# Performance work log

Hardware: AMD Instinct MI355X
Metric: run time of the kernel (lower is better)

The kernel has to match this reference:

```python
import jax, jax.numpy as jnp
import numpy as np

B, C, D, H, W = 4, 128, 24, 24, 24
P = 64


def _sparse_table(x):
    # Range-max sparse table along the last axis: level k holds max over
    # windows [i, i+2^k). Levels 0..3 (window sizes 1,2,4,8) suffice because
    # adaptive-pool region lengths are ceil(n/2) <= 12 for crop length n <= 24.
    tabs = [x]
    for k in range(1, 4):
        h = 1 << (k - 1)
        prev = tabs[-1]
        tabs.append(jnp.maximum(prev, jnp.roll(prev, -h, axis=-1)))
    return jnp.stack(tabs, 0)


def _klev(n):
    # floor(log2(n)) for n in [1, 12]
    return ((n >= 2).astype(jnp.int32) + (n >= 4).astype(jnp.int32)
            + (n >= 8).astype(jnp.int32))


def _bounds(s, e, size):
    # AdaptiveMaxPool (output size 2) region bounds along one axis.
    # crop is [s, min(e, size)); region o: [s + floor(o*n/2), s + ceil((o+1)*n/2))
    e = jnp.minimum(e, size)
    n = e - s  # crop length, always >= 2 here
    o = jnp.arange(2)
    start = s[..., None] + (o * n[..., None]) // 2
    end = s[..., None] + ((o + 1) * n[..., None] + 1) // 2
    return start, end


def _qmax(T, idx_prefix, sa, se):
    # Range max over [sa, se) along the last axis via two overlapping
    # power-of-two windows from the sparse table T ([L, ..., S]).
    k = _klev(se - sa)
    i2 = se - jnp.left_shift(1, k)
    lo = T[(k,) + idx_prefix + (Ellipsis, sa)]
    hi = T[(k,) + idx_prefix + (Ellipsis, i2)]
    return jnp.maximum(lo, hi)


def _crop_pool(fm, corners, scale):
    b, c, d, h, w = fm.shape
    p = corners.shape[1]
    # int(x/scale) with non-negative ints == floor division
    p1 = jnp.clip(corners[:, :, 0, :] // scale, 0, 21)   # [B,P,3]
    p2r = corners[:, :, 1, :] // scale
    p2 = jnp.where(p2r - p1 >= 2, p2r, p1 + 2)           # [B,P,3], p2 >= p1+2

    bi = jnp.arange(b)[:, None, None]                    # [B,1,1]
    pi = jnp.arange(p)[None, :, None]                    # [1,P,1]

    # reduce z (W axis): [B,C,D,H,W] -> [B,P,2(oz),C,D,H]
    sa, se = _bounds(p1[..., 2], p2[..., 2], w)
    r = _qmax(_sparse_table(fm), (bi,), sa, se)
    # reduce y (H axis): -> [B,P,2(oy),2(oz),C,D]
    sa, se = _bounds(p1[..., 1], p2[..., 1], h)
    r = _qmax(_sparse_table(r), (bi, pi), sa, se)
    # reduce x (D axis): -> [B,P,2(ox),2(oy),2(oz),C]
    sa, se = _bounds(p1[..., 0], p2[..., 0], d)
    r = _qmax(_sparse_table(r), (bi, pi), sa, se)
    # -> [B,P,C,2,2,2]
    return jnp.transpose(r, (0, 1, 5, 2, 3, 4))


def setup_inputs() -> dict:
    key = jax.random.key(0)
    k1, k2 = jax.random.split(key)
    fm = jax.random.normal(k1, (B, C, D, H, W), dtype=jnp.float32)
    corners = jax.random.randint(k2, (B, P, 2, 3), 0, 96, dtype=jnp.int32)
    return {"fm": fm, "corners": corners, "scale": 4}


def reference(fm, corners, scale):
    return _crop_pool(fm, corners, scale)
```

## Files before the change

### kernel.cpp

```cpp
#include <hip/hip_runtime.h>
#include <math.h>

#define Bc 4
#define Cc 128
#define Pc 64
#define PLANE 576
#define VOL   13824
#define NI    (-INFINITY)


struct Acc { float v00, v01, v10, v11; };

template<int RMODE>
__device__ __forceinline__ void upd(Acc& a, float t0, float t1) {
    if (RMODE != 1) { a.v00 = fmaxf(a.v00, t0); a.v01 = fmaxf(a.v01, t1); }
    if (RMODE != 0) { a.v10 = fmaxf(a.v10, t0); a.v11 = fmaxf(a.v11, t1); }
}

#define TREE(v, B) fmaxf(fmaxf((v).x + (B).x, (v).y + (B).y),               \
                         fmaxf((v).z + (B).z, (v).w + (B).w))

template<int RMODE>
__device__ __forceinline__ void run_seg(
    const float* __restrict__& pA, const float* __restrict__& pB, int n,
    bool c1p, bool c2p, const int fcl[3],
    const float4 B0, const float4 B1, Acc* aA, Acc* aB)
{
#pragma unroll 4
    for (int i = 0; i < n; ++i) {
        {
            float4 vA = *(const float4*)(pA + fcl[0]);
            float4 vB = *(const float4*)(pB + fcl[0]);
            upd<RMODE>(aA[0], TREE(vA, B0), TREE(vA, B1));
            upd<RMODE>(aB[0], TREE(vB, B0), TREE(vB, B1));
        }
        if (c1p) {
            float4 vA = *(const float4*)(pA + fcl[1]);
            float4 vB = *(const float4*)(pB + fcl[1]);
            upd<RMODE>(aA[1], TREE(vA, B0), TREE(vA, B1));
            upd<RMODE>(aB[1], TREE(vB, B0), TREE(vB, B1));
        }
        if (c2p) {
            float4 vA = *(const float4*)(pA + fcl[2]);
            float4 vB = *(const float4*)(pB + fcl[2]);
            upd<RMODE>(aA[2], TREE(vA, B0), TREE(vA, B1));
            upd<RMODE>(aB[2], TREE(vB, B0), TREE(vB, B1));
        }
        pA += PLANE; pB += PLANE;
    }
}

__global__ __launch_bounds__(256) void crop_pool_kernel(
    const float* __restrict__ fm, const int* __restrict__ corners,
    const int* __restrict__ scale_p, float* __restrict__ out)
{
    const int lane = threadIdx.x & 63;
    const int wid  = threadIdx.x >> 6;
    const int bp   = blockIdx.x >> 4;
    const int cg   = blockIdx.x & 15;
    const int slot = cg * 4 + wid;
    const int cA   = slot;
    const int cB   = slot + 64;
    const int b    = bp >> 6;

    const float inv = 1.0f / (float)scale_p[0];

    int s[3], e[3], m0a[3], m1a[3];
#pragma unroll
    for (int k = 0; k < 3; ++k) {
        int c0 = corners[(bp * 2 + 0) * 3 + k];
        int c1 = corners[(bp * 2 + 1) * 3 + k];
        int p1v = (int)((float)c0 * inv);
        p1v = p1v > 21 ? 21 : p1v;
        int p2v = (int)((float)c1 * inv);
        if (p2v - p1v < 2) p2v = p1v + 2;
        int ee = p2v < 24 ? p2v : 24;
        int n  = ee - p1v;
        s[k]   = __builtin_amdgcn_readfirstlane(p1v);
        e[k]   = __builtin_amdgcn_readfirstlane(ee);
        m0a[k] = __builtin_amdgcn_readfirstlane(p1v + ((n + 1) >> 1));
        m1a[k] = __builtin_amdgcn_readfirstlane(p1v + (n >> 1));
    }

    const int sh  = s[1], eh = e[1], nh = eh - sh;
    const int m0h = m0a[1], m1h = m1a[1];
    const int sw  = s[2], ew = e[2], m0w = m0a[2], m1w = m1a[2];

    const int qb = sw & ~3;
    const int Q  = ((sw & 3) + (ew - sw) + 3) >> 2;
    const int R  = 64 / Q;

    const unsigned M = (65536u + (unsigned)Q - 1) / (unsigned)Q;
    const int r = (int)(((unsigned)lane * M) >> 16);
    const int q = lane - r * Q;
    const int wbase = qb + 4 * q;

    const bool c1p = nh > R;
    const bool c2p = nh > 2 * R;

    float4 B0, B1;
    {
        int wt;
        wt = wbase + 0;
        B0.x = (wt >= sw  && wt < m0w) ? 0.0f : NI;
        B1.x = (wt >= m1w && wt < ew ) ? 0.0f : NI;
        wt = wbase + 1;
        B0.y = (wt >= sw  && wt < m0w) ? 0.0f : NI;
        B1.y = (wt >= m1w && wt < ew ) ? 0.0f : NI;
        wt = wbase + 2;
        B0.z = (wt >= sw  && wt < m0w) ? 0.0f : NI;
        B1.z = (wt >= m1w && wt < ew ) ? 0.0f : NI;
        wt = wbase + 3;
        B0.w = (wt >= sw  && wt < m0w) ? 0.0f : NI;
        B1.w = (wt >= m1w && wt < ew ) ? 0.0f : NI;
    }

    int  fcl[3];
    bool h0m[3], h1m[3];
#pragma unroll
    for (int K = 0; K < 3; ++K) {
        const int  h  = sh + K * R + r;
        const bool va = h < eh;
        const int  f  = h * 24 + wbase;
        fcl[K] = f < (PLANE - 4) ? f : (PLANE - 4);
        h0m[K] = va && (h <  m0h);
        h1m[K] = va && (h >= m1h);
    }

    Acc aA[3], aB[3];
#pragma unroll
    for (int K = 0; K < 3; ++K) {
        aA[K].v00=NI; aA[K].v01=NI; aA[K].v10=NI; aA[K].v11=NI;
        aB[K].v00=NI; aB[K].v01=NI; aB[K].v10=NI; aB[K].v11=NI;
    }

    const float* __restrict__ pA =
        fm + ((size_t)(b * Cc + cA)) * VOL + (size_t)s[0] * PLANE;
    const float* __restrict__ pB =
        fm + ((size_t)(b * Cc + cB)) * VOL + (size_t)s[0] * PLANE;

    run_seg<0>(pA, pB, m1a[0] - s[0],   c1p, c2p, fcl, B0, B1, aA, aB);
    run_seg<2>(pA, pB, m0a[0] - m1a[0], c1p, c2p, fcl, B0, B1, aA, aB);
    run_seg<1>(pA, pB, e[0]  - m0a[0],  c1p, c2p, fcl, B0, B1, aA, aB);

    float oA[8], oB[8];
#pragma unroll
    for (int j = 0; j < 8; ++j) { oA[j] = NI; oB[j] = NI; }
#pragma unroll
    for (int K = 0; K < 3; ++K) {
        if (K == 1 && !c1p) continue;
        if (K == 2 && !c2p) continue;
        oA[0] = fmaxf(oA[0], h0m[K] ? aA[K].v00 : NI);
        oA[1] = fmaxf(oA[1], h0m[K] ? aA[K].v01 : NI);
        oA[2] = fmaxf(oA[2], h1m[K] ? aA[K].v00 : NI);
        oA[3] = fmaxf(oA[3], h1m[K] ? aA[K].v01 : NI);
        oA[4] = fmaxf(oA[4], h0m[K] ? aA[K].v10 : NI);
        oA[5] = fmaxf(oA[5], h0m[K] ? aA[K].v11 : NI);
        oA[6] = fmaxf(oA[6], h1m[K] ? aA[K].v10 : NI);
        oA[7] = fmaxf(oA[7], h1m[K] ? aA[K].v11 : NI);
        oB[0] = fmaxf(oB[0], h0m[K] ? aB[K].v00 : NI);
        oB[1] = fmaxf(oB[1], h0m[K] ? aB[K].v01 : NI);
        oB[2] = fmaxf(oB[2], h1m[K] ? aB[K].v00 : NI);
        oB[3] = fmaxf(oB[3], h1m[K] ? aB[K].v01 : NI);
        oB[4] = fmaxf(oB[4], h0m[K] ? aB[K].v10 : NI);
        oB[5] = fmaxf(oB[5], h0m[K] ? aB[K].v11 : NI);
        oB[6] = fmaxf(oB[6], h1m[K] ? aB[K].v10 : NI);
        oB[7] = fmaxf(oB[7], h1m[K] ? aB[K].v11 : NI);
    }

    const bool lo = lane < 32;
    float x[8];
#pragma unroll
    for (int j = 0; j < 8; ++j) {
        float keep = lo ? oA[j] : oB[j];
        float send = lo ? oB[j] : oA[j];
        x[j] = fmaxf(keep, __shfl_xor(send, 32));
    }
    const bool b0 = lane & 1, b1 = lane & 2, b2 = lane & 4;
    float m0_ = fmaxf(b0 ? x[1] : x[0], __shfl_xor(b0 ? x[0] : x[1], 1));
    float m1_ = fmaxf(b0 ? x[3] : x[2], __shfl_xor(b0 ? x[2] : x[3], 1));
    float m2_ = fmaxf(b0 ? x[5] : x[4], __shfl_xor(b0 ? x[4] : x[5], 1));
    float m3_ = fmaxf(b0 ? x[7] : x[6], __shfl_xor(b0 ? x[6] : x[7], 1));
    float n0_ = fmaxf(b1 ? m1_ : m0_, __shfl_xor(b1 ? m0_ : m1_, 2));
    float n1_ = fmaxf(b1 ? m3_ : m2_, __shfl_xor(b1 ? m2_ : m3_, 2));
    float v   = fmaxf(b2 ? n1_ : n0_, __shfl_xor(b2 ? n0_ : n1_, 4));
    v = fmaxf(v, __shfl_xor(v, 8));
    v = fmaxf(v, __shfl_xor(v, 16));

    if ((lane & 31) < 8) {
        const int cc = lo ? cA : cB;
        out[((size_t)bp * Cc + cc) * 8 + (lane & 7)] = v;
    }
}

extern "C" void kernel_launch(void* const* d_in, const int* in_sizes, int n_in,
                              void* d_out, int out_size, void* d_ws, size_t ws_size,
                              hipStream_t stream) {
    const float* fm      = (const float*)d_in[0];
    const int*   corners = (const int*)d_in[1];
    const int*   scale   = (const int*)d_in[2];
    float*       out     = (float*)d_out;

    dim3 grid(Bc * Pc * 16);
    dim3 block(256);
    crop_pool_kernel<<<grid, block, 0, stream>>>(fm, corners, scale, out);
}
```

Before: 23.64 us.

## Split wavefront halves across alternating depth slices when the crop fits

When the H-W crop fits within three row groups of 32 lanes, the two wavefront halves take even and odd depth slices, halving the serial depth loop. The three templated depth segments are replaced by a single loop that uses per-slice predicated masks for the two output regions. The last slice is clamped, so an odd trailing iteration repeats a load. This costs extra select instructions and can leave more lanes idle in the HW mapping, but shortens the serial latency chain of loads per wave.

```diff
diff --git a/kernel.cpp b/kernel.cpp
--- a/kernel.cpp
+++ b/kernel.cpp
@@ -9,46 +9,8 @@
 #define NI    (-INFINITY)
 
 
-struct Acc { float v00, v01, v10, v11; };
-
-template<int RMODE>
-__device__ __forceinline__ void upd(Acc& a, float t0, float t1) {
-    if (RMODE != 1) { a.v00 = fmaxf(a.v00, t0); a.v01 = fmaxf(a.v01, t1); }
-    if (RMODE != 0) { a.v10 = fmaxf(a.v10, t0); a.v11 = fmaxf(a.v11, t1); }
-}
-
 #define TREE(v, B) fmaxf(fmaxf((v).x + (B).x, (v).y + (B).y),               \
                          fmaxf((v).z + (B).z, (v).w + (B).w))
-
-template<int RMODE>
-__device__ __forceinline__ void run_seg(
-    const float* __restrict__& pA, const float* __restrict__& pB, int n,
-    bool c1p, bool c2p, const int fcl[3],
-    const float4 B0, const float4 B1, Acc* aA, Acc* aB)
-{
-#pragma unroll 4
-    for (int i = 0; i < n; ++i) {
-        {
-            float4 vA = *(const float4*)(pA + fcl[0]);
-            float4 vB = *(const float4*)(pB + fcl[0]);
-            upd<RMODE>(aA[0], TREE(vA, B0), TREE(vA, B1));
-            upd<RMODE>(aB[0], TREE(vB, B0), TREE(vB, B1));
-        }
-        if (c1p) {
-            float4 vA = *(const float4*)(pA + fcl[1]);
-            float4 vB = *(const float4*)(pB + fcl[1]);
-            upd<RMODE>(aA[1], TREE(vA, B0), TREE(vA, B1));
-            upd<RMODE>(aB[1], TREE(vB, B0), TREE(vB, B1));
-        }
-        if (c2p) {
-            float4 vA = *(const float4*)(pA + fcl[2]);
-            float4 vB = *(const float4*)(pB + fcl[2]);
-            upd<RMODE>(aA[2], TREE(vA, B0), TREE(vA, B1));
-            upd<RMODE>(aB[2], TREE(vB, B0), TREE(vB, B1));
-        }
-        pA += PLANE; pB += PLANE;
-    }
-}
 
 __global__ __launch_bounds__(256) void crop_pool_kernel(
     const float* __restrict__ fm, const int* __restrict__ corners,
@@ -82,21 +44,28 @@
         m1a[k] = __builtin_amdgcn_readfirstlane(p1v + (n >> 1));
     }
 
-    const int sh  = s[1], eh = e[1], nh = eh - sh;
+    const int sd = s[0], ed = e[0], m0d = m0a[0], m1d = m1a[0];
+    const int sh = s[1], eh = e[1], nh = eh - sh;
     const int m0h = m0a[1], m1h = m1a[1];
-    const int sw  = s[2], ew = e[2], m0w = m0a[2], m1w = m1a[2];
+    const int sw = s[2], ew = e[2], m0w = m0a[2], m1w = m1a[2];
 
     const int qb = sw & ~3;
     const int Q  = ((sw & 3) + (ew - sw) + 3) >> 2;
-    const int R  = 64 / Q;
 
     const unsigned M = (65536u + (unsigned)Q - 1) / (unsigned)Q;
-    const int r = (int)(((unsigned)lane * M) >> 16);
-    const int q = lane - r * Q;
+    const int R2 = (int)((32u * M) >> 16);
+    const bool s2ok = nh <= 3 * R2;
+    const int S     = s2ok ? 2 : 1;
+    const int Reff  = s2ok ? R2 : (int)((64u * M) >> 16);
+    const int lm    = s2ok ? (lane & 31) : lane;
+    const int halfv = s2ok ? (lane >> 5) : 0;
+
+    const int r = (int)(((unsigned)lm * M) >> 16);
+    const int q = lm - r * Q;
     const int wbase = qb + 4 * q;
 
-    const bool c1p = nh > R;
-    const bool c2p = nh > 2 * R;
+    const bool c1p = nh > Reff;
+    const bool c2p = nh > 2 * Reff;
 
     float4 B0, B1;
     {
@@ -119,29 +88,52 @@
     bool h0m[3], h1m[3];
 #pragma unroll
     for (int K = 0; K < 3; ++K) {
-        const int  h  = sh + K * R + r;
-        const bool va = h < eh;
-        const int  f  = h * 24 + wbase;
+        const int  hrow = K * Reff + r;
+        const int  h    = sh + hrow;
+        const bool va   = hrow < nh;
+        const int  f    = h * 24 + wbase;
         fcl[K] = f < (PLANE - 4) ? f : (PLANE - 4);
         h0m[K] = va && (h <  m0h);
         h1m[K] = va && (h >= m1h);
     }
 
-    Acc aA[3], aB[3];
+    struct Acc { float v00, v01, v10, v11; } aA[3], aB[3];
 #pragma unroll
     for (int K = 0; K < 3; ++K) {
         aA[K].v00=NI; aA[K].v01=NI; aA[K].v10=NI; aA[K].v11=NI;
         aB[K].v00=NI; aB[K].v01=NI; aB[K].v10=NI; aB[K].v11=NI;
     }
 
-    const float* __restrict__ pA =
-        fm + ((size_t)(b * Cc + cA)) * VOL + (size_t)s[0] * PLANE;
-    const float* __restrict__ pB =
-        fm + ((size_t)(b * Cc + cB)) * VOL + (size_t)s[0] * PLANE;
+    const float* __restrict__ pA0 = fm + ((size_t)(b * Cc + cA)) * VOL;
+    const float* __restrict__ pB0 = fm + ((size_t)(b * Cc + cB)) * VOL;
+    const int emax = ed - 1;
 
-    run_seg<0>(pA, pB, m1a[0] - s[0],   c1p, c2p, fcl, B0, B1, aA, aB);
-    run_seg<2>(pA, pB, m0a[0] - m1a[0], c1p, c2p, fcl, B0, B1, aA, aB);
-    run_seg<1>(pA, pB, e[0]  - m0a[0],  c1p, c2p, fcl, B0, B1, aA, aB);
+    for (int d = sd; d < ed; d += S) {
+        const int  dh  = d + halfv;
+        const int  dcl = dh < emax ? dh : emax;
+        const bool f0  = dcl <  m0d;
+        const bool f1  = dcl >= m1d;
+        const int  ob  = dcl * PLANE;
+
+#define CH(K) {                                                             \
+        float4 vA = *(const float4*)(pA0 + ob + fcl[K]);                    \
+        float4 vB = *(const float4*)(pB0 + ob + fcl[K]);                    \
+        float t0A = TREE(vA, B0), t1A = TREE(vA, B1);                       \
+        float t0B = TREE(vB, B0), t1B = TREE(vB, B1);                       \
+        aA[K].v00 = fmaxf(aA[K].v00, f0 ? t0A : NI);                        \
+        aA[K].v01 = fmaxf(aA[K].v01, f0 ? t1A : NI);                        \
+        aA[K].v10 = fmaxf(aA[K].v10, f1 ? t0A : NI);                        \
+        aA[K].v11 = fmaxf(aA[K].v11, f1 ? t1A : NI);                        \
+        aB[K].v00 = fmaxf(aB[K].v00, f0 ? t0B : NI);                        \
+        aB[K].v01 = fmaxf(aB[K].v01, f0 ? t1B : NI);                        \
+        aB[K].v10 = fmaxf(aB[K].v10, f1 ? t0B : NI);                        \
+        aB[K].v11 = fmaxf(aB[K].v11, f1 ? t1B : NI);                        \
+    }
+        CH(0)
+        if (c1p) CH(1)
+        if (c2p) CH(2)
+#undef CH
+    }
 
     float oA[8], oB[8];
 #pragma unroll
```

After: 21.69 us. 8.3% less time.

## Process four channels per wave and halve the grid to amortize setup

Applied to the files above, without the earlier changes.

Each wave now handles four channels in two sequential passes instead of two, and the grid shrinks from 16 to 8 blocks per (batch, box). The per-box bound computation, masks and lane mapping are computed once and reused across both passes, so the setup cost is spread over more work. The unroll pragma on the inner depth loop is dropped, and R is now computed with a reciprocal multiply instead of an integer divide. The tradeoffs are fewer waves in flight for hiding memory latency and longer per-thread serial work.

```diff
diff --git a/kernel.cpp b/kernel.cpp
--- a/kernel.cpp
+++ b/kernel.cpp
@@ -26,7 +26,6 @@
     bool c1p, bool c2p, const int fcl[3],
     const float4 B0, const float4 B1, Acc* aA, Acc* aB)
 {
-#pragma unroll 4
     for (int i = 0; i < n; ++i) {
         {
             float4 vA = *(const float4*)(pA + fcl[0]);
@@ -50,83 +49,12 @@
     }
 }
 
-__global__ __launch_bounds__(256) void crop_pool_kernel(
-    const float* __restrict__ fm, const int* __restrict__ corners,
-    const int* __restrict__ scale_p, float* __restrict__ out)
+__device__ __forceinline__ void run_pass(
+    const float* __restrict__ pA, const float* __restrict__ pB,
+    int n0, int n1, int n2, bool c1p, bool c2p, const int fcl[3],
+    const float4 B0, const float4 B1,
+    const bool h0m[3], const bool h1m[3], bool lo, float x[8])
 {
-    const int lane = threadIdx.x & 63;
-    const int wid  = threadIdx.x >> 6;
-    const int bp   = blockIdx.x >> 4;
-    const int cg   = blockIdx.x & 15;
-    const int slot = cg * 4 + wid;
-    const int cA   = slot;
-    const int cB   = slot + 64;
-    const int b    = bp >> 6;
-
-    const float inv = 1.0f / (float)scale_p[0];
-
-    int s[3], e[3], m0a[3], m1a[3];
-#pragma unroll
-    for (int k = 0; k < 3; ++k) {
-        int c0 = corners[(bp * 2 + 0) * 3 + k];
-        int c1 = corners[(bp * 2 + 1) * 3 + k];
-        int p1v = (int)((float)c0 * inv);
-        p1v = p1v > 21 ? 21 : p1v;
-        int p2v = (int)((float)c1 * inv);
-        if (p2v - p1v < 2) p2v = p1v + 2;
-        int ee = p2v < 24 ? p2v : 24;
-        int n  = ee - p1v;
-        s[k]   = __builtin_amdgcn_readfirstlane(p1v);
-        e[k]   = __builtin_amdgcn_readfirstlane(ee);
-        m0a[k] = __builtin_amdgcn_readfirstlane(p1v + ((n + 1) >> 1));
-        m1a[k] = __builtin_amdgcn_readfirstlane(p1v + (n >> 1));
-    }
-
-    const int sh  = s[1], eh = e[1], nh = eh - sh;
-    const int m0h = m0a[1], m1h = m1a[1];
-    const int sw  = s[2], ew = e[2], m0w = m0a[2], m1w = m1a[2];
-
-    const int qb = sw & ~3;
-    const int Q  = ((sw & 3) + (ew - sw) + 3) >> 2;
-    const int R  = 64 / Q;
-
-    const unsigned M = (65536u + (unsigned)Q - 1) / (unsigned)Q;
-    const int r = (int)(((unsigned)lane * M) >> 16);
-    const int q = lane - r * Q;
-    const int wbase = qb + 4 * q;
-
-    const bool c1p = nh > R;
-    const bool c2p = nh > 2 * R;
-
-    float4 B0, B1;
-    {
-        int wt;
-        wt = wbase + 0;
-        B0.x = (wt >= sw  && wt < m0w) ? 0.0f : NI;
-        B1.x = (wt >= m1w && wt < ew ) ? 0.0f : NI;
-        wt = wbase + 1;
-        B0.y = (wt >= sw  && wt < m0w) ? 0.0f : NI;
-        B1.y = (wt >= m1w && wt < ew ) ? 0.0f : NI;
-        wt = wbase + 2;
-        B0.z = (wt >= sw  && wt < m0w) ? 0.0f : NI;
-        B1.z = (wt >= m1w && wt < ew ) ? 0.0f : NI;
-        wt = wbase + 3;
-        B0.w = (wt >= sw  && wt < m0w) ? 0.0f : NI;
-        B1.w = (wt >= m1w && wt < ew ) ? 0.0f : NI;
-    }
-
-    int  fcl[3];
-    bool h0m[3], h1m[3];
-#pragma unroll
-    for (int K = 0; K < 3; ++K) {
-        const int  h  = sh + K * R + r;
-        const bool va = h < eh;
-        const int  f  = h * 24 + wbase;
-        fcl[K] = f < (PLANE - 4) ? f : (PLANE - 4);
-        h0m[K] = va && (h <  m0h);
-        h1m[K] = va && (h >= m1h);
-    }
-
     Acc aA[3], aB[3];
 #pragma unroll
     for (int K = 0; K < 3; ++K) {
@@ -134,14 +62,9 @@
         aB[K].v00=NI; aB[K].v01=NI; aB[K].v10=NI; aB[K].v11=NI;
     }
 
-    const float* __restrict__ pA =
-        fm + ((size_t)(b * Cc + cA)) * VOL + (size_t)s[0] * PLANE;
-    const float* __restrict__ pB =
-        fm + ((size_t)(b * Cc + cB)) * VOL + (size_t)s[0] * PLANE;
-
-    run_seg<0>(pA, pB, m1a[0] - s[0],   c1p, c2p, fcl, B0, B1, aA, aB);
-    run_seg<2>(pA, pB, m0a[0] - m1a[0], c1p, c2p, fcl, B0, B1, aA, aB);
-    run_seg<1>(pA, pB, e[0]  - m0a[0],  c1p, c2p, fcl, B0, B1, aA, aB);
+    run_seg<0>(pA, pB, n0, c1p, c2p, fcl, B0, B1, aA, aB);
+    run_seg<2>(pA, pB, n1, c1p, c2p, fcl, B0, B1, aA, aB);
+    run_seg<1>(pA, pB, n2, c1p, c2p, fcl, B0, B1, aA, aB);
 
     float oA[8], oB[8];
 #pragma unroll
@@ -167,29 +90,125 @@
         oB[6] = fmaxf(oB[6], h1m[K] ? aB[K].v10 : NI);
         oB[7] = fmaxf(oB[7], h1m[K] ? aB[K].v11 : NI);
     }
-
-    const bool lo = lane < 32;
-    float x[8];
 #pragma unroll
     for (int j = 0; j < 8; ++j) {
         float keep = lo ? oA[j] : oB[j];
         float send = lo ? oB[j] : oA[j];
         x[j] = fmaxf(keep, __shfl_xor(send, 32));
     }
+}
+
+__device__ __forceinline__ float oct_reduce32(const float x[8], int lane) {
     const bool b0 = lane & 1, b1 = lane & 2, b2 = lane & 4;
-    float m0_ = fmaxf(b0 ? x[1] : x[0], __shfl_xor(b0 ? x[0] : x[1], 1));
-    float m1_ = fmaxf(b0 ? x[3] : x[2], __shfl_xor(b0 ? x[2] : x[3], 1));
-    float m2_ = fmaxf(b0 ? x[5] : x[4], __shfl_xor(b0 ? x[4] : x[5], 1));
-    float m3_ = fmaxf(b0 ? x[7] : x[6], __shfl_xor(b0 ? x[6] : x[7], 1));
-    float n0_ = fmaxf(b1 ? m1_ : m0_, __shfl_xor(b1 ? m0_ : m1_, 2));
-    float n1_ = fmaxf(b1 ? m3_ : m2_, __shfl_xor(b1 ? m2_ : m3_, 2));
-    float v   = fmaxf(b2 ? n1_ : n0_, __shfl_xor(b2 ? n0_ : n1_, 4));
+    float m0 = fmaxf(b0 ? x[1] : x[0], __shfl_xor(b0 ? x[0] : x[1], 1));
+    float m1 = fmaxf(b0 ? x[3] : x[2], __shfl_xor(b0 ? x[2] : x[3], 1));
+    float m2 = fmaxf(b0 ? x[5] : x[4], __shfl_xor(b0 ? x[4] : x[5], 1));
+    float m3 = fmaxf(b0 ? x[7] : x[6], __shfl_xor(b0 ? x[6] : x[7], 1));
+    float n0 = fmaxf(b1 ? m1 : m0, __shfl_xor(b1 ? m0 : m1, 2));
+    float n1 = fmaxf(b1 ? m3 : m2, __shfl_xor(b1 ? m2 : m3, 2));
+    float v  = fmaxf(b2 ? n1 : n0, __shfl_xor(b2 ? n0 : n1, 4));
     v = fmaxf(v, __shfl_xor(v, 8));
     v = fmaxf(v, __shfl_xor(v, 16));
+    return v;
+}
+
+__global__ __launch_bounds__(256) void crop_pool_kernel(
+    const float* __restrict__ fm, const int* __restrict__ corners,
+    const int* __restrict__ scale_p, float* __restrict__ out)
+{
+    const int lane = threadIdx.x & 63;
+    const int wid  = threadIdx.x >> 6;
+    const int bp   = blockIdx.x >> 3;
+    const int slot = (blockIdx.x & 7) * 4 + wid;
+    const int b    = bp >> 6;
+
+    const float inv = 1.0f / (float)scale_p[0];
+
+    int s[3], e[3], m0a[3], m1a[3];
+#pragma unroll
+    for (int k = 0; k < 3; ++k) {
+        int c0 = corners[(bp * 2 + 0) * 3 + k];
+        int c1 = corners[(bp * 2 + 1) * 3 + k];
+        int p1v = (int)((float)c0 * inv);
+        p1v = p1v > 21 ? 21 : p1v;
+        int p2v = (int)((float)c1 * inv);
+        if (p2v - p1v < 2) p2v = p1v + 2;
+        int ee = p2v < 24 ? p2v : 24;
+        int n  = ee - p1v;
+        s[k]   = __builtin_amdgcn_readfirstlane(p1v);
+        e[k]   = __builtin_amdgcn_readfirstlane(ee);
+        m0a[k] = __builtin_amdgcn_readfirstlane(p1v + ((n + 1) >> 1));
+        m1a[k] = __builtin_amdgcn_readfirstlane(p1v + (n >> 1));
+    }
+
+    const int n0 = m1a[0] - s[0];
+    const int n1 = m0a[0] - m1a[0];
+    const int n2 = e[0] - m0a[0];
+    const int sh = s[1], eh = e[1], nh = eh - sh;
+    const int m0h = m0a[1], m1h = m1a[1];
+    const int sw = s[2], ew = e[2], m0w = m0a[2], m1w = m1a[2];
+
+    const int qb = sw & ~3;
+    const int Q  = ((sw & 3) + (ew - sw) + 3) >> 2;
+    const unsigned M = (65536u + (unsigned)Q - 1) / (unsigned)Q;
+    const int R = (int)((64u * M) >> 16);
+
+    const int r = (int)(((unsigned)lane * M) >> 16);
+    const int q = lane - r * Q;
+    const int wbase = qb + 4 * q;
+
+    const bool c1p = nh > R;
+    const bool c2p = nh > 2 * R;
+
+    float4 B0, B1;
+    {
+        int wt;
+        wt = wbase + 0;
+        B0.x = (wt >= sw  && wt < m0w) ? 0.0f : NI;
+        B1.x = (wt >= m1w && wt < ew ) ? 0.0f : NI;
+        wt = wbase + 1;
+        B0.y = (wt >= sw  && wt < m0w) ? 0.0f : NI;
+        B1.y = (wt >= m1w && wt < ew ) ? 0.0f : NI;
+        wt = wbase + 2;
+        B0.z = (wt >= sw  && wt < m0w) ? 0.0f : NI;
+        B1.z = (wt >= m1w && wt < ew ) ? 0.0f : NI;
+        wt = wbase + 3;
+        B0.w = (wt >= sw  && wt < m0w) ? 0.0f : NI;
+        B1.w = (wt >= m1w && wt < ew ) ? 0.0f : NI;
+    }
+
+    int  fcl[3];
+    bool h0m[3], h1m[3];
+#pragma unroll
+    for (int K = 0; K < 3; ++K) {
+        const int  hrow = K * R + r;
+        const int  h    = sh + hrow;
+        const bool va   = hrow < nh;
+        const int  f    = h * 24 + wbase;
+        fcl[K] = f < (PLANE - 4) ? f : (PLANE - 4);
+        h0m[K] = va && (h <  m0h);
+        h1m[K] = va && (h >= m1h);
+    }
+
+    const bool   lo   = lane < 32;
+    const size_t doff = (size_t)s[0] * PLANE;
+    const float* base = fm + (size_t)b * Cc * VOL + doff;
+
+    float x0[8];
+    run_pass(base + (size_t)(slot     ) * VOL, base + (size_t)(slot + 64) * VOL,
+             n0, n1, n2, c1p, c2p, fcl, B0, B1, h0m, h1m, lo, x0);
+    float x1[8];
+    run_pass(base + (size_t)(slot + 32) * VOL, base + (size_t)(slot + 96) * VOL,
+             n0, n1, n2, c1p, c2p, fcl, B0, B1, h0m, h1m, lo, x1);
+
+    const float v0 = oct_reduce32(x0, lane);
+    const float v1 = oct_reduce32(x1, lane);
 
     if ((lane & 31) < 8) {
-        const int cc = lo ? cA : cB;
-        out[((size_t)bp * Cc + cc) * 8 + (lane & 7)] = v;
+        const int c0 = lo ? slot      : slot + 64;
+        const int c1 = lo ? slot + 32 : slot + 96;
+        out[((size_t)bp * Cc + c0) * 8 + (lane & 7)] = v0;
+        out[((size_t)bp * Cc + c1) * 8 + (lane & 7)] = v1;
     }
 }
 
@@ -201,7 +220,7 @@
     const int*   scale   = (const int*)d_in[2];
     float*       out     = (float*)d_out;
 
-    dim3 grid(Bc * Pc * 16);
+    dim3 grid(Bc * Pc * 8);
     dim3 block(256);
     crop_pool_kernel<<<grid, block, 0, stream>>>(fm, corners, scale, out);
 }
```

Result: slower. 24.21 us (+2.4%).
